# Optimization experiments

Hardware: AMD Instinct MI355X
Metric: run time of the kernel (lower is better)

Reference implementation:

```python
import jax, jax.numpy as jnp
import numpy as np

IN_CH, OUT_CH, K, STRIDE = 128, 256, 3, 1

def setup_inputs() -> dict:
    key = jax.random.key(0)
    kx, kw = jax.random.split(key)
    x = jax.random.normal(kx, (32, IN_CH, 56, 56), dtype=jnp.float32)
    # xavier_uniform: bound = sqrt(6 / (fan_in + fan_out)), fans include receptive field
    fan_in = IN_CH * K * K
    fan_out = OUT_CH * K * K
    bound = float(np.sqrt(6.0 / (fan_in + fan_out)))
    weight = jax.random.uniform(kw, (OUT_CH, IN_CH, K, K), dtype=jnp.float32,
                                minval=-bound, maxval=bound)
    bias = jnp.zeros((OUT_CH,), dtype=jnp.float32)
    return {"x": x, "weight": weight, "bias": bias}

def reference(x, weight, bias):
    # VALID (no-padding) conv, stride STRIDE, NCHW layout, OIHW kernel
    out = jax.lax.conv_general_dilated(
        x, weight,
        window_strides=(STRIDE, STRIDE),
        padding="VALID",
        dimension_numbers=("NCHW", "OIHW", "NCHW"))
    return out + bias[None, :, None, None]
```

## Files before the change

kernel.cpp:

```cpp
#include <hip/hip_runtime.h>
#include <hip/hip_bf16.h>
#include <stdint.h>

#define NB    32
#define CIN   128
#define HIN   56
#define HW    (HIN*HIN)
#define OCH   256
#define OHW   54
#define SPB   (OHW*OHW)
#define KSZ   (CIN*9)
#define BM    256
#define BN    192
#define BK    64
#define NKS   (KSZ/BK)
#define TOTC  (NB*SPB)
#define NT    486
#define GRAN  ((BM+BN)*8)

typedef __attribute__((ext_vector_type(8))) short bf16x8;
typedef __attribute__((ext_vector_type(4))) float f32x4;

typedef __attribute__((address_space(1))) const uint32_t g_u32;
typedef __attribute__((address_space(3))) uint32_t l_u32;
static __device__ __forceinline__ void gl_lds16(const void* g, void* l) {
    __builtin_amdgcn_global_load_lds((g_u32*)g, (l_u32*)l, 16, 0, 0);
}

__global__ void xpose_cast(const float* __restrict__ x, __hip_bfloat16* __restrict__ xt) {
    __shared__ float tile[32][33];
    const int hw0 = blockIdx.x * 32;
    const int c0  = blockIdx.y * 32;
    const int n   = blockIdx.z;
    const int tx = threadIdx.x, ty = threadIdx.y;
    const float* xp = x + ((size_t)n*CIN + c0)*HW + hw0;
    #pragma unroll
    for (int i = ty; i < 32; i += 8)
        tile[i][tx] = xp[(size_t)i*HW + tx];
    __syncthreads();
    const int t = ty*32 + tx;
    const int hwl = t >> 3, q = t & 7;
    ushort4 v;
    v.x = __bfloat16_as_ushort(__float2bfloat16(tile[q*4+0][hwl]));
    v.y = __bfloat16_as_ushort(__float2bfloat16(tile[q*4+1][hwl]));
    v.z = __bfloat16_as_ushort(__float2bfloat16(tile[q*4+2][hwl]));
    v.w = __bfloat16_as_ushort(__float2bfloat16(tile[q*4+3][hwl]));
    __hip_bfloat16* op = xt + ((size_t)n*HW + hw0 + hwl)*CIN + c0 + q*4;
    *(ushort4*)op = v;
}

__global__ void wcast(const float* __restrict__ w, __hip_bfloat16* __restrict__ wt) {
    int tid = blockIdx.x*256 + threadIdx.x;
    if (tid >= OCH*KSZ) return;
    int oc = tid / KSZ, r = tid % KSZ;
    int pos = r >> 7, ic = r & 127;
    wt[tid] = __float2bfloat16(w[((size_t)(oc*CIN + ic))*9 + pos]);
}

__global__ __launch_bounds__(512, 2)
void conv_mfma(const __hip_bfloat16* __restrict__ xt,
               const __hip_bfloat16* __restrict__ wt,
               const float* __restrict__ bias,
               float* __restrict__ out) {
    __shared__ uint4 smem[2*GRAN];

    const int t = threadIdx.x;
    const int orig = blockIdx.x;
    const int xcd = orig & 7;
    const int tile = (xcd < 6 ? xcd*61 : 6*61 + (xcd-6)*60) + (orig >> 3);

    const int lane = t & 63, wid = t >> 6;
    const int wm = wid >> 2, wn = wid & 3;
    const int lr = lane & 15, lq = lane >> 4;

    const __hip_bfloat16* aptr[4];
    #pragma unroll
    for (int i = 0; i < 4; ++i) {
        int q = i*512 + t;
        int row = q >> 3, j = q & 7;
        int ls = j ^ (row & 7);
        aptr[i] = wt + (size_t)row*KSZ + ls*8;
    }
    const __hip_bfloat16* bptr[3];
    #pragma unroll
    for (int i = 0; i < 3; ++i) {
        int q = i*512 + t;
        int row = q >> 3, j = q & 7;
        int ls = j ^ (row & 7);
        int colg = tile*BN + row;
        int n = colg / SPB, rem = colg - n*SPB;
        int oh = rem / OHW, ow = rem - oh*OHW;
        bptr[i] = xt + ((size_t)(n*HIN + oh)*HIN + ow)*CIN + ls*8;
    }

    auto issueT = [&](int ks) {
        uint4* dst = smem + (ks & 1)*GRAN;
        const int aoff = ks*BK;
        const int pos = ks >> 1;
        const int kh = pos / 3, kw = pos - kh*3;
        const int boff = (kh*HIN + kw)*CIN + (ks & 1)*64;
        #pragma unroll
        for (int i = 0; i < 4; ++i) gl_lds16(aptr[i] + aoff, dst + i*512 + t);
        #pragma unroll
        for (int i = 0; i < 3; ++i) gl_lds16(bptr[i] + boff, dst + 2048 + i*512 + t);
    };

    int ao[8], bo[3];
    #pragma unroll
    for (int mi = 0; mi < 8; ++mi) {
        int ra = wm*128 + mi*16 + lr;
        ao[mi] = ra*8 + (lq ^ (ra & 7));
    }
    #pragma unroll
    for (int ni = 0; ni < 3; ++ni) {
        int rb = wn*48 + ni*16 + lr;
        bo[ni] = 2048 + rb*8 + (lq ^ (rb & 7));
    }

    f32x4 acc[8][3];
    #pragma unroll
    for (int i = 0; i < 8; ++i)
        #pragma unroll
        for (int j = 0; j < 3; ++j)
            acc[i][j] = (f32x4){0.f, 0.f, 0.f, 0.f};

    #define MFMA_BF16 __builtin_amdgcn_mfma_f32_16x16x32_bf16
    #define MFMA12(AARR, MIB, BARR) \
        __builtin_amdgcn_s_setprio(1); \
        _Pragma("unroll") \
        for (int ii = 0; ii < 4; ++ii) \
            _Pragma("unroll") \
            for (int ni = 0; ni < 3; ++ni) \
                acc[(MIB)+ii][ni] = MFMA_BF16(AARR[ii], BARR[ni], acc[(MIB)+ii][ni], 0, 0, 0); \
        __builtin_amdgcn_s_setprio(0);

    issueT(0);
    asm volatile("s_waitcnt vmcnt(0)" ::: "memory");
    __builtin_amdgcn_s_barrier();
    __builtin_amdgcn_sched_barrier(0);

    for (int ks = 0; ks < NKS; ++ks) {
        const uint4* buf = smem + (ks & 1)*GRAN;
        bf16x8 a[4], a2[4], b[3];

        #pragma unroll
        for (int mi = 0; mi < 4; ++mi) a[mi] = *(bf16x8*)&buf[ao[mi]];
        #pragma unroll
        for (int ni = 0; ni < 3; ++ni) b[ni] = *(bf16x8*)&buf[bo[ni]];
        if (ks + 1 < NKS) issueT(ks + 1);
        #pragma unroll
        for (int mi = 0; mi < 4; ++mi) a2[mi] = *(bf16x8*)&buf[ao[4 + mi]];

        asm volatile("s_waitcnt lgkmcnt(4)" ::: "memory");
        __builtin_amdgcn_sched_barrier(0);
        MFMA12(a, 0, b)
        asm volatile("s_waitcnt lgkmcnt(0)" ::: "memory");
        __builtin_amdgcn_sched_barrier(0);
        MFMA12(a2, 4, b)

        #pragma unroll
        for (int mi = 0; mi < 4; ++mi) a[mi] = *(bf16x8*)&buf[ao[mi] ^ 4];
        #pragma unroll
        for (int ni = 0; ni < 3; ++ni) b[ni] = *(bf16x8*)&buf[bo[ni] ^ 4];
        #pragma unroll
        for (int mi = 0; mi < 4; ++mi) a2[mi] = *(bf16x8*)&buf[ao[4 + mi] ^ 4];

        asm volatile("s_waitcnt lgkmcnt(4)" ::: "memory");
        __builtin_amdgcn_sched_barrier(0);
        MFMA12(a, 0, b)
        asm volatile("s_waitcnt lgkmcnt(0)" ::: "memory");
        __builtin_amdgcn_sched_barrier(0);
        MFMA12(a2, 4, b)

        if (ks + 1 < NKS) {
            asm volatile("s_waitcnt vmcnt(0)" ::: "memory");
            __builtin_amdgcn_s_barrier();
            __builtin_amdgcn_sched_barrier(0);
        }
    }

    __syncthreads();

    float (*eps)[196] = (float (*)[196])smem;
    const int cl4 = (t % 48) * 4;
    const int rsub = t / 48;
    const int colg = tile*BN + cl4;
    const int nn = colg / SPB;
    const int sp = colg - nn*SPB;
    #pragma unroll
    for (int h = 0; h < 4; ++h) {
        if (wm == (h >> 1)) {
            const int mib = (h & 1) * 4;
            #pragma unroll
            for (int ii = 0; ii < 4; ++ii) {
                int rl = ii*16 + lq*4;
                #pragma unroll
                for (int ni = 0; ni < 3; ++ni) {
                    int cl = wn*48 + ni*16 + lr;
                    #pragma unroll
                    for (int r = 0; r < 4; ++r)
                        eps[rl + r][cl] = acc[mib + ii][ni][r];
                }
            }
        }
        __syncthreads();
        if (t < 384) {
            #pragma unroll
            for (int pass = 0; pass < 8; ++pass) {
                int rl = pass*8 + rsub;
                int rg = h*64 + rl;
                f32x4 v = *(f32x4*)&eps[rl][cl4];
                v = v + bias[rg];
                *(f32x4*)&out[((size_t)nn*OCH + rg)*SPB + sp] = v;
            }
        }
        __syncthreads();
    }
}

__global__ void conv_naive(const float* __restrict__ x, const float* __restrict__ w,
                           const float* __restrict__ bias, float* __restrict__ out) {
    size_t tid = (size_t)blockIdx.x*256 + threadIdx.x;
    const size_t total = (size_t)NB*OCH*SPB;
    if (tid >= total) return;
    int col = (int)(tid % SPB);
    int oc  = (int)((tid / SPB) % OCH);
    int n   = (int)(tid / ((size_t)SPB*OCH));
    int oh = col / OHW, ow = col % OHW;
    float s = bias[oc];
    for (int ic = 0; ic < CIN; ++ic)
        #pragma unroll
        for (int kh = 0; kh < 3; ++kh)
            #pragma unroll
            for (int kw = 0; kw < 3; ++kw)
                s += x[((size_t)(n*CIN+ic)*HIN + oh+kh)*HIN + ow+kw]
                   * w[((size_t)(oc*CIN+ic)*3 + kh)*3 + kw];
    out[tid] = s;
}

extern "C" void kernel_launch(void* const* d_in, const int* in_sizes, int n_in,
                              void* d_out, int out_size, void* d_ws, size_t ws_size,
                              hipStream_t stream) {
    const float* x    = (const float*)d_in[0];
    const float* w    = (const float*)d_in[1];
    const float* bias = (const float*)d_in[2];
    float* out = (float*)d_out;

    const size_t xt_bytes = (size_t)NB*HW*CIN*sizeof(__hip_bfloat16);
    const size_t wt_bytes = (size_t)OCH*KSZ*sizeof(__hip_bfloat16);

    if (ws_size >= xt_bytes + wt_bytes) {
        __hip_bfloat16* xt  = (__hip_bfloat16*)d_ws;
        __hip_bfloat16* wtp = (__hip_bfloat16*)((char*)d_ws + xt_bytes);
        hipLaunchKernelGGL(xpose_cast, dim3(HW/32, CIN/32, NB), dim3(32, 8), 0, stream, x, xt);
        hipLaunchKernelGGL(wcast, dim3((OCH*KSZ + 255)/256), dim3(256), 0, stream, w, wtp);
        hipLaunchKernelGGL(conv_mfma, dim3(NT), dim3(512), 0, stream, xt, wtp, bias, out);
    } else {
        size_t total = (size_t)NB*OCH*SPB;
        hipLaunchKernelGGL(conv_naive, dim3((unsigned)((total + 255)/256)), dim3(256), 0, stream,
                           x, w, bias, out);
    }
}
```

Baseline: 82.73 us.

## Widen N tile to 384 and load weights directly into registers

The output-column tile grows from 192 to 384, which halves the block count to 243. Weight (A) fragments now come straight from global memory into registers with a prefetch of the next K-step, and only the input (B) tile is staged in LDS through global_load_lds. This is meant to cut LDS traffic and the per-block overhead of loading weights, and to raise MFMA work per barrier. In exchange it doubles the accumulator registers (8x6 tiles), which risks register pressure and lower occupancy. It also leaves only 243 blocks for the CUs, and the epilogue is split into two column halves.

```diff
diff --git a/kernel.cpp b/kernel.cpp
--- a/kernel.cpp
+++ b/kernel.cpp
@@ -11,12 +11,12 @@
 #define SPB   (OHW*OHW)
 #define KSZ   (CIN*9)
 #define BM    256
-#define BN    192
+#define BN    384
 #define BK    64
 #define NKS   (KSZ/BK)
 #define TOTC  (NB*SPB)
-#define NT    486
-#define GRAN  ((BM+BN)*8)
+#define NT    243
+#define BGRAN (BN*8)
 
 typedef __attribute__((ext_vector_type(8))) short bf16x8;
 typedef __attribute__((ext_vector_type(4))) float f32x4;
@@ -62,118 +62,103 @@
                const __hip_bfloat16* __restrict__ wt,
                const float* __restrict__ bias,
                float* __restrict__ out) {
-    __shared__ uint4 smem[2*GRAN];
+    __shared__ uint4 smem[2*BGRAN];
 
     const int t = threadIdx.x;
     const int orig = blockIdx.x;
     const int xcd = orig & 7;
-    const int tile = (xcd < 6 ? xcd*61 : 6*61 + (xcd-6)*60) + (orig >> 3);
+    const int tile = (xcd < 3 ? xcd*31 : 3*31 + (xcd-3)*30) + (orig >> 3);
 
     const int lane = t & 63, wid = t >> 6;
     const int wm = wid >> 2, wn = wid & 3;
     const int lr = lane & 15, lq = lane >> 4;
 
-    const __hip_bfloat16* aptr[4];
-    #pragma unroll
-    for (int i = 0; i < 4; ++i) {
+    const __hip_bfloat16* abase = wt + (size_t)(wm*128 + lr)*KSZ + lq*8;
+
+    const __hip_bfloat16* bsrc[6];
+    #pragma unroll
+    for (int i = 0; i < 6; ++i) {
         int q = i*512 + t;
-        int row = q >> 3, j = q & 7;
-        int ls = j ^ (row & 7);
-        aptr[i] = wt + (size_t)row*KSZ + ls*8;
-    }
-    const __hip_bfloat16* bptr[3];
-    #pragma unroll
-    for (int i = 0; i < 3; ++i) {
-        int q = i*512 + t;
-        int row = q >> 3, j = q & 7;
-        int ls = j ^ (row & 7);
-        int colg = tile*BN + row;
+        int col = q >> 3, j = q & 7;
+        int ls = j ^ (col & 7);
+        int colg = tile*BN + col;
         int n = colg / SPB, rem = colg - n*SPB;
         int oh = rem / OHW, ow = rem - oh*OHW;
-        bptr[i] = xt + ((size_t)(n*HIN + oh)*HIN + ow)*CIN + ls*8;
-    }
-
-    auto issueT = [&](int ks) {
-        uint4* dst = smem + (ks & 1)*GRAN;
-        const int aoff = ks*BK;
+        bsrc[i] = xt + ((size_t)(n*HIN + oh)*HIN + ow)*CIN + ls*8;
+    }
+
+    auto stageB = [&](int ks) {
+        uint4* dst = smem + (ks & 1)*BGRAN;
         const int pos = ks >> 1;
         const int kh = pos / 3, kw = pos - kh*3;
         const int boff = (kh*HIN + kw)*CIN + (ks & 1)*64;
         #pragma unroll
-        for (int i = 0; i < 4; ++i) gl_lds16(aptr[i] + aoff, dst + i*512 + t);
-        #pragma unroll
-        for (int i = 0; i < 3; ++i) gl_lds16(bptr[i] + boff, dst + 2048 + i*512 + t);
+        for (int i = 0; i < 6; ++i) gl_lds16(bsrc[i] + boff, dst + i*512 + t);
     };
 
-    int ao[8], bo[3];
-    #pragma unroll
-    for (int mi = 0; mi < 8; ++mi) {
-        int ra = wm*128 + mi*16 + lr;
-        ao[mi] = ra*8 + (lq ^ (ra & 7));
-    }
-    #pragma unroll
-    for (int ni = 0; ni < 3; ++ni) {
-        int rb = wn*48 + ni*16 + lr;
-        bo[ni] = 2048 + rb*8 + (lq ^ (rb & 7));
-    }
-
-    f32x4 acc[8][3];
+    int bo[6];
+    #pragma unroll
+    for (int ni = 0; ni < 6; ++ni) {
+        int c = wn*96 + ni*16 + lr;
+        bo[ni] = c*8 + (lq ^ (c & 7));
+    }
+
+    f32x4 acc[8][6];
     #pragma unroll
     for (int i = 0; i < 8; ++i)
         #pragma unroll
-        for (int j = 0; j < 3; ++j)
+        for (int j = 0; j < 6; ++j)
             acc[i][j] = (f32x4){0.f, 0.f, 0.f, 0.f};
 
     #define MFMA_BF16 __builtin_amdgcn_mfma_f32_16x16x32_bf16
-    #define MFMA12(AARR, MIB, BARR) \
+    #define LDA8(ARR, KOFF) \
+        _Pragma("unroll") \
+        for (int mi = 0; mi < 8; ++mi) \
+            ARR[mi] = *(const bf16x8*)(abase + (size_t)mi*16*KSZ + (KOFF));
+    #define MFMA48(AARR, BARR) \
         __builtin_amdgcn_s_setprio(1); \
         _Pragma("unroll") \
-        for (int ii = 0; ii < 4; ++ii) \
+        for (int mi = 0; mi < 8; ++mi) \
             _Pragma("unroll") \
-            for (int ni = 0; ni < 3; ++ni) \
-                acc[(MIB)+ii][ni] = MFMA_BF16(AARR[ii], BARR[ni], acc[(MIB)+ii][ni], 0, 0, 0); \
+            for (int ni = 0; ni < 6; ++ni) \
+                acc[mi][ni] = MFMA_BF16(AARR[mi], BARR[ni], acc[mi][ni], 0, 0, 0); \
         __builtin_amdgcn_s_setprio(0);
 
-    issueT(0);
+    bf16x8 a0[8], a1[8];
+
+    LDA8(a0, 0)
+    LDA8(a1, 32)
+    stageB(0);
     asm volatile("s_waitcnt vmcnt(0)" ::: "memory");
     __builtin_amdgcn_s_barrier();
     __builtin_amdgcn_sched_barrier(0);
 
     for (int ks = 0; ks < NKS; ++ks) {
-        const uint4* buf = smem + (ks & 1)*GRAN;
-        bf16x8 a[4], a2[4], b[3];
-
-        #pragma unroll
-        for (int mi = 0; mi < 4; ++mi) a[mi] = *(bf16x8*)&buf[ao[mi]];
-        #pragma unroll
-        for (int ni = 0; ni < 3; ++ni) b[ni] = *(bf16x8*)&buf[bo[ni]];
-        if (ks + 1 < NKS) issueT(ks + 1);
-        #pragma unroll
-        for (int mi = 0; mi < 4; ++mi) a2[mi] = *(bf16x8*)&buf[ao[4 + mi]];
-
-        asm volatile("s_waitcnt lgkmcnt(4)" ::: "memory");
+        const uint4* Bb = smem + (ks & 1)*BGRAN;
+        const bool pf = (ks + 1 < NKS);
+        bf16x8 b0[6], b1[6];
+        #pragma unroll
+        for (int ni = 0; ni < 6; ++ni) b0[ni] = *(const bf16x8*)&Bb[bo[ni]];
+        #pragma unroll
+        for (int ni = 0; ni < 6; ++ni) b1[ni] = *(const bf16x8*)&Bb[bo[ni] ^ 4];
+
+        asm volatile("s_waitcnt lgkmcnt(6)" ::: "memory");
         __builtin_amdgcn_sched_barrier(0);
-        MFMA12(a, 0, b)
+        MFMA48(a0, b0)
+
+        if (pf) { LDA8(a0, (ks+1)*BK) }
+        if (pf) stageB(ks + 1);
+
         asm volatile("s_waitcnt lgkmcnt(0)" ::: "memory");
+        if (pf) asm volatile("s_waitcnt vmcnt(14)" ::: "memory");
+        else    asm volatile("s_waitcnt vmcnt(0)" ::: "memory");
         __builtin_amdgcn_sched_barrier(0);
-        MFMA12(a2, 4, b)
-
-        #pragma unroll
-        for (int mi = 0; mi < 4; ++mi) a[mi] = *(bf16x8*)&buf[ao[mi] ^ 4];
-        #pragma unroll
-        for (int ni = 0; ni < 3; ++ni) b[ni] = *(bf16x8*)&buf[bo[ni] ^ 4];
-        #pragma unroll
-        for (int mi = 0; mi < 4; ++mi) a2[mi] = *(bf16x8*)&buf[ao[4 + mi] ^ 4];
-
-        asm volatile("s_waitcnt lgkmcnt(4)" ::: "memory");
-        __builtin_amdgcn_sched_barrier(0);
-        MFMA12(a, 0, b)
-        asm volatile("s_waitcnt lgkmcnt(0)" ::: "memory");
-        __builtin_amdgcn_sched_barrier(0);
-        MFMA12(a2, 4, b)
-
-        if (ks + 1 < NKS) {
-            asm volatile("s_waitcnt vmcnt(0)" ::: "memory");
+        MFMA48(a1, b1)
+
+        if (pf) { LDA8(a1, (ks+1)*BK + 32) }
+
+        if (pf) {
+            asm volatile("s_waitcnt vmcnt(8)" ::: "memory");
             __builtin_amdgcn_s_barrier();
             __builtin_amdgcn_sched_barrier(0);
         }
@@ -184,37 +169,40 @@
     float (*eps)[196] = (float (*)[196])smem;
     const int cl4 = (t % 48) * 4;
     const int rsub = t / 48;
-    const int colg = tile*BN + cl4;
-    const int nn = colg / SPB;
-    const int sp = colg - nn*SPB;
     #pragma unroll
     for (int h = 0; h < 4; ++h) {
-        if (wm == (h >> 1)) {
-            const int mib = (h & 1) * 4;
-            #pragma unroll
-            for (int ii = 0; ii < 4; ++ii) {
-                int rl = ii*16 + lq*4;
+        #pragma unroll
+        for (int half = 0; half < 2; ++half) {
+            if (wm == (h >> 1) && (wn >> 1) == half) {
+                const int mib = (h & 1) * 4;
                 #pragma unroll
-                for (int ni = 0; ni < 3; ++ni) {
-                    int cl = wn*48 + ni*16 + lr;
+                for (int ii = 0; ii < 4; ++ii) {
+                    int rl = ii*16 + lq*4;
                     #pragma unroll
-                    for (int r = 0; r < 4; ++r)
-                        eps[rl + r][cl] = acc[mib + ii][ni][r];
+                    for (int ni = 0; ni < 6; ++ni) {
+                        int cl = (wn & 1)*96 + ni*16 + lr;
+                        #pragma unroll
+                        for (int r = 0; r < 4; ++r)
+                            eps[rl + r][cl] = acc[mib + ii][ni][r];
+                    }
                 }
             }
+            __syncthreads();
+            if (t < 384) {
+                const int colg = tile*BN + half*192 + cl4;
+                const int nn = colg / SPB;
+                const int sp = colg - nn*SPB;
+                #pragma unroll
+                for (int pass = 0; pass < 8; ++pass) {
+                    int rl = pass*8 + rsub;
+                    int rg = h*64 + rl;
+                    f32x4 v = *(f32x4*)&eps[rl][cl4];
+                    v = v + bias[rg];
+                    *(f32x4*)&out[((size_t)nn*OCH + rg)*SPB + sp] = v;
+                }
+            }
+            __syncthreads();
         }
-        __syncthreads();
-        if (t < 384) {
-            #pragma unroll
-            for (int pass = 0; pass < 8; ++pass) {
-                int rl = pass*8 + rsub;
-                int rg = h*64 + rl;
-                f32x4 v = *(f32x4*)&eps[rl][cl4];
-                v = v + bias[rg];
-                *(f32x4*)&out[((size_t)nn*OCH + rg)*SPB + sp] = v;
-            }
-        }
-        __syncthreads();
     }
 }
 
```

Result: slower. 328.0 us (+296.4%).
